# Performance work log

Hardware: AMD Instinct MI355X
Metric: run time of the kernel (lower is better)

Reference implementation:

```python
import jax, jax.numpy as jnp
import numpy as np

NUM_HEADS = 8
EPS = 1e-12  # torch F.normalize eps


def _l2norm(t):
    n = jnp.linalg.norm(t, axis=-1, keepdims=True)
    return t / jnp.maximum(n, EPS)


def setup_inputs() -> dict:
    key = jax.random.key(0)
    k1, k2, k3 = jax.random.split(key, 3)
    B, T, N, D = 16, 12, 1024, 128
    x = jax.random.normal(k1, (B, T, N, D), dtype=jnp.float32)
    # Linear(model_dim, 3*model_dim, bias=False): stored as (D, 3D) for x @ W
    W_qkv = jax.random.normal(k2, (D, 3 * D), dtype=jnp.float32) * (1.0 / np.sqrt(D))
    W_out = jax.random.normal(k3, (D, D), dtype=jnp.float32) * (1.0 / np.sqrt(D))
    b_out = jnp.zeros((D,), dtype=jnp.float32)
    return {"x": x, "W_qkv": W_qkv, "W_out": W_out, "b_out": b_out}


def reference(x, W_qkv, W_out, b_out):
    B, T, N, D = x.shape
    H = NUM_HEADS
    hd = D // H
    qkv = x @ W_qkv                                  # (B,T,N,3D)
    q, k, v = jnp.split(qkv, 3, axis=-1)
    # split heads + flatten (B,T) -> b = B*T, matching torch stack/flatten
    qs = _l2norm(q.reshape(B * T, N, H, hd))          # (b,N,H,m)
    ks = _l2norm(k.reshape(B * T, N, H, hd))
    vs = v.reshape(B * T, N, H, hd)
    # linear attention: running kv sum + normalizer
    kvs = jnp.einsum('blhm,blhd->bhmd', ks, vs)       # (b,H,m,d)
    attn_num = jnp.einsum('bnhm,bhmd->bnhd', qs, kvs) + N * vs
    ks_sum = jnp.sum(ks, axis=1)                      # (b,H,m)
    normalizer = jnp.einsum('bnhm,bhm->bnh', qs, ks_sum)[..., None] + N
    out = attn_num / normalizer                       # (b,N,H,d)
    out = out.reshape(B, T, N, D)
    return out @ W_out + b_out
```

## Files before the change

### kernel.cpp

```cpp
#include <hip/hip_runtime.h>

#define NBATCH 192
#define SEQ    1024
#define DIM    128
#define NH     8
#define EPS    1e-12f

typedef short bf16x8 __attribute__((ext_vector_type(8)));
typedef float f32x4  __attribute__((ext_vector_type(4)));

#define KVS_F  393216
#define ZERO_F 417792

static __device__ __forceinline__ unsigned short f2bf(float f) {
    unsigned u = __builtin_bit_cast(unsigned, f);
    u += 0x7fff + ((u >> 16) & 1);
    return (unsigned short)(u >> 16);
}

template <int CTRL>
static __device__ __forceinline__ float dpp_add(float v) {
    int j = __builtin_amdgcn_mov_dpp(__builtin_bit_cast(int, v), CTRL, 0xf, 0xf, false);
    return v + __builtin_bit_cast(float, j);
}
static __device__ __forceinline__ float r16sum(float v) {
    v = dpp_add<0xB1>(v);
    v = dpp_add<0x4E>(v);
    v = dpp_add<0x141>(v);
    v = dpp_add<0x140>(v);
    return v;
}

static __device__ __forceinline__ int strip_addr(int row, int el) {
    return row * 32 + ((((el >> 3) ^ (row & 3)) << 3) | (el & 7));
}

static __device__ __forceinline__ uint2 pack4(float a, float b, float c, float d) {
    uint2 r;
    r.x = (unsigned)f2bf(a) | ((unsigned)f2bf(b) << 16);
    r.y = (unsigned)f2bf(c) | ((unsigned)f2bf(d) << 16);
    return r;
}

static __device__ __forceinline__ bf16x8 cvt8(float4 a, float4 b) {
    bf16x8 r;
    r[0] = (short)f2bf(a.x); r[1] = (short)f2bf(a.y); r[2] = (short)f2bf(a.z); r[3] = (short)f2bf(a.w);
    r[4] = (short)f2bf(b.x); r[5] = (short)f2bf(b.y); r[6] = (short)f2bf(b.z); r[7] = (short)f2bf(b.w);
    return r;
}

static __device__ __forceinline__ bf16x8 gfrag(const unsigned short* __restrict__ wT,
                                               int ct, int ks, int lane) {
    return *reinterpret_cast<const bf16x8*>(wT + ((ct * 4 + ks) * 64 + lane) * 8);
}

__global__ __launch_bounds__(256) void k0_prep(const float* __restrict__ Wqkv,
                                               const float* __restrict__ Wout,
                                               unsigned short* __restrict__ wsWT) {
    int i = blockIdx.x * 256 + threadIdx.x;
    int which = i >> 14, e = i & 16383;
    int j = e & 7, f = e >> 3;
    int n15 = f & 15, q = (f >> 4) & 3, ks = (f >> 6) & 3, ct = f >> 8;
    int k = ks * 32 + q * 8 + j, n = ct * 16 + n15;
    float v = (which < 3) ? Wqkv[k * 384 + which * 128 + n] : Wout[k * 128 + n];
    wsWT[i] = f2bf(v);
}

__global__ __launch_bounds__(512, 4) void k1_kv(const float* __restrict__ x,
                                                const unsigned short* __restrict__ wsWT,
                                                float* __restrict__ kvs_ws,
                                                float* __restrict__ kssum_ws) {
    __shared__ float redf[16384];
    __shared__ unsigned short strips[8192];
    int t = threadIdx.x, w = t >> 6, lane = t & 63, q = lane >> 4, n15 = lane & 15;
    int b = blockIdx.x >> 2, seg = blockIdx.x & 3;
    const unsigned short* wkT = wsWT + 16384;
    const unsigned short* wvT = wsWT + 32768;
    unsigned short* knS = strips + w * 1024;
    unsigned short* vS  = knS + 512;

    bf16x8 ah[2][4];
#pragma unroll
    for (int rs = 0; rs < 2; ++rs) {
        int row = seg * 256 + w * 32 + rs * 16 + n15;
        const float* xr = x + (size_t)(b * SEQ + row) * DIM;
#pragma unroll
        for (int ks = 0; ks < 4; ++ks) {
            float4 p0 = *reinterpret_cast<const float4*>(xr + ks * 32 + q * 8);
            float4 p1 = *reinterpret_cast<const float4*>(xr + ks * 32 + q * 8 + 4);
            ah[rs][ks] = cvt8(p0, p1);
        }
    }

#pragma unroll 1
    for (int ct = 0; ct < 8; ++ct) {
        f32x4 ka[2] = {(f32x4){0,0,0,0}, (f32x4){0,0,0,0}};
        f32x4 va[2] = {(f32x4){0,0,0,0}, (f32x4){0,0,0,0}};
#pragma unroll
        for (int ks = 0; ks < 4; ++ks) {
            bf16x8 kb = gfrag(wkT, ct, ks, lane);
            bf16x8 vb = gfrag(wvT, ct, ks, lane);
#pragma unroll
            for (int rs = 0; rs < 2; ++rs) {
                ka[rs] = __builtin_amdgcn_mfma_f32_16x16x32_bf16(ah[rs][ks], kb, ka[rs], 0, 0, 0);
                va[rs] = __builtin_amdgcn_mfma_f32_16x16x32_bf16(ah[rs][ks], vb, va[rs], 0, 0, 0);
            }
        }
        float ksum = 0.f;
#pragma unroll
        for (int rs = 0; rs < 2; ++rs) {
            float kn[4];
#pragma unroll
            for (int r = 0; r < 4; ++r) {
                float val = ka[rs][r];
                float ssq = r16sum(val * val);
                float di  = 1.0f / fmaxf(sqrtf(ssq), EPS);
                kn[r] = val * di;
                ksum += kn[r];
            }
            *reinterpret_cast<uint2*>(knS + strip_addr(n15, rs * 16 + q * 4)) =
                pack4(kn[0], kn[1], kn[2], kn[3]);
            *reinterpret_cast<uint2*>(vS + strip_addr(n15, rs * 16 + q * 4)) =
                pack4(va[rs][0], va[rs][1], va[rs][2], va[rs][3]);
        }
        bf16x8 aK = *reinterpret_cast<const bf16x8*>(knS + strip_addr(n15, q * 8));
        bf16x8 bV = *reinterpret_cast<const bf16x8*>(vS + strip_addr(n15, q * 8));
        f32x4 kacc = __builtin_amdgcn_mfma_f32_16x16x32_bf16(aK, bV, (f32x4){0,0,0,0}, 0, 0, 0);
#pragma unroll
        for (int r = 0; r < 4; ++r)
            redf[w * 2048 + ct * 256 + (q * 4 + r) * 16 + n15] = kacc[r];
        float s = ksum;
        s += __shfl_xor(s, 16); s += __shfl_xor(s, 32);
        if (lane < 16) atomicAdd(&kssum_ws[b * 128 + ct * 16 + n15], s);
    }

    __syncthreads();
#pragma unroll
    for (int i = 0; i < 4; ++i) {
        int el = i * 512 + t;
        float s = 0.f;
#pragma unroll
        for (int ww = 0; ww < 8; ++ww) s += redf[ww * 2048 + el];
        atomicAdd(&kvs_ws[b * 2048 + el], s);
    }
}

__global__ __launch_bounds__(512, 4) void k2_out(const float* __restrict__ x,
                                                 const unsigned short* __restrict__ wsWT,
                                                 const float* __restrict__ kvs_ws,
                                                 const float* __restrict__ kssum_ws,
                                                 const float* __restrict__ bout,
                                                 float* __restrict__ out) {
    __shared__ unsigned short lds[40960];
    unsigned short* kvsT   = lds;
    unsigned short* strips = lds + 4096;
    unsigned short* tile   = lds + 8192;
    int t = threadIdx.x, w = t >> 6, lane = t & 63, q = lane >> 4, n15 = lane & 15;
    int b = blockIdx.x >> 2, seg = blockIdx.x & 3, rowbase = seg * 256;
    const unsigned short* wqT = wsWT;
    const unsigned short* wvT = wsWT + 32768;
    const unsigned short* woT = wsWT + 49152;

    {
        int row = t >> 2, part = t & 3, h = row >> 4, d = row & 15;
        unsigned es[8];
#pragma unroll
        for (int j = 0; j < 8; j += 2) {
            int m0 = part * 8 + j;
            unsigned lo = (m0     < 16) ? f2bf(kvs_ws[b * 2048 + h * 256 + m0 * 16 + d])      : 0;
            unsigned hi = (m0 + 1 < 16) ? f2bf(kvs_ws[b * 2048 + h * 256 + (m0 + 1) * 16 + d]) : 0;
            es[j] = lo | (hi << 16);
        }
        uint4 v = {es[0], es[2], es[4], es[6]};
        *reinterpret_cast<uint4*>(kvsT + row * 32 + ((part ^ (row & 3)) << 3)) = v;
    }

    bf16x8 ah[2][4];
#pragma unroll
    for (int rs = 0; rs < 2; ++rs) {
        int row = rowbase + w * 32 + rs * 16 + n15;
        const float* xr = x + (size_t)(b * SEQ + row) * DIM;
#pragma unroll
        for (int ks = 0; ks < 4; ++ks) {
            float4 p0 = *reinterpret_cast<const float4*>(xr + ks * 32 + q * 8);
            float4 p1 = *reinterpret_cast<const float4*>(xr + ks * 32 + q * 8 + 4);
            ah[rs][ks] = cvt8(p0, p1);
        }
    }

    unsigned short* myS = strips + w * 512;
    unsigned short* tw  = tile + w * 4096;
    {
        uint2 z = {0, 0};
        *reinterpret_cast<uint2*>(myS + strip_addr(n15, 16 + q * 4)) = z;
    }
    __syncthreads();

#pragma unroll
    for (int rs = 0; rs < 2; ++rs)
#pragma unroll 1
        for (int h = 0; h < 8; ++h) {
            float kssh = kssum_ws[b * 128 + h * 16 + n15];
            f32x4 qa = (f32x4){0,0,0,0};
            f32x4 va = (f32x4){0,0,0,0};
#pragma unroll
            for (int ks = 0; ks < 4; ++ks) {
                bf16x8 qb = gfrag(wqT, h, ks, lane);
                bf16x8 vb = gfrag(wvT, h, ks, lane);
                qa = __builtin_amdgcn_mfma_f32_16x16x32_bf16(ah[rs][ks], qb, qa, 0, 0, 0);
                va = __builtin_amdgcn_mfma_f32_16x16x32_bf16(ah[rs][ks], vb, va, 0, 0, 0);
            }
            float pv[4];
#pragma unroll
            for (int r = 0; r < 4; ++r) {
                float val = qa[r];
                float ssq = r16sum(val * val);
                float tt  = r16sum(val * kssh);
                float di  = 1.0f / fmaxf(sqrtf(ssq), EPS);
                float inv = 1.0f / (tt * di + (float)SEQ);
                pv[r] = val * di * inv;
                va[r] *= (float)SEQ * inv;
            }
#pragma unroll
            for (int r = 0; r < 4; ++r)
                myS[strip_addr(q * 4 + r, n15)] = f2bf(pv[r]);
            bf16x8 aq = *reinterpret_cast<const bf16x8*>(myS + strip_addr(n15, q * 8));
            bf16x8 bk = *reinterpret_cast<const bf16x8*>(kvsT + strip_addr(h * 16 + n15, q * 8));
            va = __builtin_amdgcn_mfma_f32_16x16x32_bf16(aq, bk, va, 0, 0, 0);
#pragma unroll
            for (int r = 0; r < 4; ++r) {
                int rt = rs * 16 + q * 4 + r;
                int colg = h * 2 + (n15 >> 3);
                tw[rt * 128 + (((colg ^ (rt & 15)) << 3) | (n15 & 7))] = f2bf(va[r]);
            }
        }

    bf16x8 ap[2][4];
#pragma unroll
    for (int rs = 0; rs < 2; ++rs)
#pragma unroll
        for (int ks = 0; ks < 4; ++ks) {
            int rt = rs * 16 + n15;
            ap[rs][ks] = *reinterpret_cast<const bf16x8*>(
                tw + rt * 128 + ((((ks << 2) + q) ^ (rt & 15)) << 3));
        }
#pragma unroll 1
    for (int ct = 0; ct < 8; ++ct) {
        f32x4 o0 = (f32x4){0,0,0,0};
        f32x4 o1 = (f32x4){0,0,0,0};
#pragma unroll
        for (int ks = 0; ks < 4; ++ks) {
            bf16x8 bb = gfrag(woT, ct, ks, lane);
            o0 = __builtin_amdgcn_mfma_f32_16x16x32_bf16(ap[0][ks], bb, o0, 0, 0, 0);
            o1 = __builtin_amdgcn_mfma_f32_16x16x32_bf16(ap[1][ks], bb, o1, 0, 0, 0);
        }
        float bo = bout[ct * 16 + n15];
#pragma unroll
        for (int r = 0; r < 4; ++r) {
            int row0 = rowbase + w * 32 + q * 4 + r;
            out[(size_t)(b * SEQ + row0) * DIM + ct * 16 + n15]      = o0[r] + bo;
            out[(size_t)(b * SEQ + row0 + 16) * DIM + ct * 16 + n15] = o1[r] + bo;
        }
    }
}

extern "C" void kernel_launch(void* const* d_in, const int* in_sizes, int n_in,
                              void* d_out, int out_size, void* d_ws, size_t ws_size,
                              hipStream_t stream) {
    const float* x    = (const float*)d_in[0];
    const float* Wqkv = (const float*)d_in[1];
    const float* Wout = (const float*)d_in[2];
    const float* bout = (const float*)d_in[3];
    float* out = (float*)d_out;

    float* kvs_ws   = (float*)d_ws;
    float* kssum_ws = kvs_ws + KVS_F;
    unsigned short* wsWT = (unsigned short*)((char*)d_ws + (size_t)ZERO_F * 4);

    hipMemsetAsync(d_ws, 0, (size_t)ZERO_F * 4, stream);
    k0_prep<<<dim3(256), dim3(256), 0, stream>>>(Wqkv, Wout, wsWT);
    k1_kv<<<dim3(768), dim3(512), 0, stream>>>(x, wsWT, kvs_ws, kssum_ws);
    k2_out<<<dim3(768), dim3(512), 0, stream>>>(x, wsWT, kvs_ws, kssum_ws, bout, out);
}
```

Before: 282.2 us.

## Shrink LDS footprint in both kernels to raise occupancy to six blocks

```diff
diff --git a/kernel.cpp b/kernel.cpp
--- a/kernel.cpp
+++ b/kernel.cpp
@@ -66,11 +66,11 @@
     wsWT[i] = f2bf(v);
 }
 
-__global__ __launch_bounds__(512, 4) void k1_kv(const float* __restrict__ x,
+__global__ __launch_bounds__(512, 6) void k1_kv(const float* __restrict__ x,
                                                 const unsigned short* __restrict__ wsWT,
                                                 float* __restrict__ kvs_ws,
                                                 float* __restrict__ kssum_ws) {
-    __shared__ float redf[16384];
+    __shared__ float kvsagg[2048];
     __shared__ unsigned short strips[8192];
     int t = threadIdx.x, w = t >> 6, lane = t & 63, q = lane >> 4, n15 = lane & 15;
     int b = blockIdx.x >> 2, seg = blockIdx.x & 3;
@@ -79,6 +79,9 @@
     unsigned short* knS = strips + w * 1024;
     unsigned short* vS  = knS + 512;
 
+#pragma unroll
+    for (int i = 0; i < 4; ++i) kvsagg[i * 512 + t] = 0.0f;
+
     bf16x8 ah[2][4];
 #pragma unroll
     for (int rs = 0; rs < 2; ++rs) {
@@ -91,6 +94,7 @@
             ah[rs][ks] = cvt8(p0, p1);
         }
     }
+    __syncthreads();
 
 #pragma unroll 1
     for (int ct = 0; ct < 8; ++ct) {
@@ -128,7 +132,7 @@
         f32x4 kacc = __builtin_amdgcn_mfma_f32_16x16x32_bf16(aK, bV, (f32x4){0,0,0,0}, 0, 0, 0);
 #pragma unroll
         for (int r = 0; r < 4; ++r)
-            redf[w * 2048 + ct * 256 + (q * 4 + r) * 16 + n15] = kacc[r];
+            atomicAdd(&kvsagg[ct * 256 + (q * 4 + r) * 16 + n15], kacc[r]);
         float s = ksum;
         s += __shfl_xor(s, 16); s += __shfl_xor(s, 32);
         if (lane < 16) atomicAdd(&kssum_ws[b * 128 + ct * 16 + n15], s);
@@ -138,20 +142,17 @@
 #pragma unroll
     for (int i = 0; i < 4; ++i) {
         int el = i * 512 + t;
-        float s = 0.f;
-#pragma unroll
-        for (int ww = 0; ww < 8; ++ww) s += redf[ww * 2048 + el];
-        atomicAdd(&kvs_ws[b * 2048 + el], s);
-    }
-}
-
-__global__ __launch_bounds__(512, 4) void k2_out(const float* __restrict__ x,
+        atomicAdd(&kvs_ws[b * 2048 + el], kvsagg[el]);
+    }
+}
+
+__global__ __launch_bounds__(512, 6) void k2_out(const float* __restrict__ x,
                                                  const unsigned short* __restrict__ wsWT,
                                                  const float* __restrict__ kvs_ws,
                                                  const float* __restrict__ kssum_ws,
                                                  const float* __restrict__ bout,
                                                  float* __restrict__ out) {
-    __shared__ unsigned short lds[40960];
+    __shared__ unsigned short lds[24576];
     unsigned short* kvsT   = lds;
     unsigned short* strips = lds + 4096;
     unsigned short* tile   = lds + 8192;
@@ -189,7 +190,7 @@
     }
 
     unsigned short* myS = strips + w * 512;
-    unsigned short* tw  = tile + w * 4096;
+    unsigned short* tw  = tile + w * 2048;
     {
         uint2 z = {0, 0};
         *reinterpret_cast<uint2*>(myS + strip_addr(n15, 16 + q * 4)) = z;
@@ -197,7 +198,7 @@
     __syncthreads();
 
 #pragma unroll
-    for (int rs = 0; rs < 2; ++rs)
+    for (int rs = 0; rs < 2; ++rs) {
 #pragma unroll 1
         for (int h = 0; h < 8; ++h) {
             float kssh = kssum_ws[b * 128 + h * 16 + n15];
@@ -229,37 +230,31 @@
             va = __builtin_amdgcn_mfma_f32_16x16x32_bf16(aq, bk, va, 0, 0, 0);
 #pragma unroll
             for (int r = 0; r < 4; ++r) {
-                int rt = rs * 16 + q * 4 + r;
+                int rt = q * 4 + r;
                 int colg = h * 2 + (n15 >> 3);
-                tw[rt * 128 + (((colg ^ (rt & 15)) << 3) | (n15 & 7))] = f2bf(va[r]);
-            }
-        }
-
-    bf16x8 ap[2][4];
-#pragma unroll
-    for (int rs = 0; rs < 2; ++rs)
-#pragma unroll
-        for (int ks = 0; ks < 4; ++ks) {
-            int rt = rs * 16 + n15;
-            ap[rs][ks] = *reinterpret_cast<const bf16x8*>(
-                tw + rt * 128 + ((((ks << 2) + q) ^ (rt & 15)) << 3));
-        }
+                tw[rt * 128 + (((colg ^ rt) << 3) | (n15 & 7))] = f2bf(va[r]);
+            }
+        }
+
+        bf16x8 ap[4];
+#pragma unroll
+        for (int ks = 0; ks < 4; ++ks)
+            ap[ks] = *reinterpret_cast<const bf16x8*>(
+                tw + n15 * 128 + ((((ks << 2) + q) ^ n15) << 3));
 #pragma unroll 1
-    for (int ct = 0; ct < 8; ++ct) {
-        f32x4 o0 = (f32x4){0,0,0,0};
-        f32x4 o1 = (f32x4){0,0,0,0};
-#pragma unroll
-        for (int ks = 0; ks < 4; ++ks) {
-            bf16x8 bb = gfrag(woT, ct, ks, lane);
-            o0 = __builtin_amdgcn_mfma_f32_16x16x32_bf16(ap[0][ks], bb, o0, 0, 0, 0);
-            o1 = __builtin_amdgcn_mfma_f32_16x16x32_bf16(ap[1][ks], bb, o1, 0, 0, 0);
-        }
-        float bo = bout[ct * 16 + n15];
-#pragma unroll
-        for (int r = 0; r < 4; ++r) {
-            int row0 = rowbase + w * 32 + q * 4 + r;
-            out[(size_t)(b * SEQ + row0) * DIM + ct * 16 + n15]      = o0[r] + bo;
-            out[(size_t)(b * SEQ + row0 + 16) * DIM + ct * 16 + n15] = o1[r] + bo;
+        for (int ct = 0; ct < 8; ++ct) {
+            f32x4 oa = (f32x4){0,0,0,0};
+#pragma unroll
+            for (int ks = 0; ks < 4; ++ks) {
+                bf16x8 bb = gfrag(woT, ct, ks, lane);
+                oa = __builtin_amdgcn_mfma_f32_16x16x32_bf16(ap[ks], bb, oa, 0, 0, 0);
+            }
+            float bo = bout[ct * 16 + n15];
+#pragma unroll
+            for (int r = 0; r < 4; ++r) {
+                int row = rowbase + w * 32 + rs * 16 + q * 4 + r;
+                out[(size_t)(b * SEQ + row) * DIM + ct * 16 + n15] = oa[r] + bo;
+            }
         }
     }
 }
```

Result: slower. 331.3 us (+17.4%).
